# Optimization experiments

Measured on AMD Instinct MI355X. Metric: run time of the kernel, lower is better.

Reference implementation:

```python
import jax, jax.numpy as jnp
import numpy as np

B, N, D, H = 8, 2048, 512, 8  # batch, seq (incl. CLS), emb_dim, heads


def setup_inputs() -> dict:
    key = jax.random.key(0)
    kx, km, k1, k2, k3, k4 = jax.random.split(key, 6)
    x = jax.random.normal(kx, (B, N, D), dtype=jnp.float32)
    # mask covers the N-1 non-CLS tokens; forward pads a leading True for CLS
    mask = jax.random.bernoulli(km, p=0.9, shape=(B, N - 1))
    s = 0.02
    Wqkv = jax.random.normal(k1, (D, 3 * D), dtype=jnp.float32) * s
    bqkv = jax.random.normal(k2, (3 * D,), dtype=jnp.float32) * s
    Wout = jax.random.normal(k3, (D, D), dtype=jnp.float32) * s
    bout = jax.random.normal(k4, (D,), dtype=jnp.float32) * s
    return {"x": x, "mask": mask, "Wqkv": Wqkv, "bqkv": bqkv,
            "Wout": Wout, "bout": bout, "num_heads": H}


def reference(x, mask, Wqkv, bqkv, Wout, bout, num_heads):
    b, n, d = x.shape
    h = num_heads
    dh = d // h
    scale = d ** (-0.5)  # NOTE: module scales by emb_dim^-0.5, not head_dim^-0.5

    qkv = x @ Wqkv + bqkv                      # [b, n, 3d]
    q, k, v = jnp.split(qkv, 3, axis=-1)
    def to_heads(t):
        return t.reshape(b, n, h, dh).transpose(0, 2, 1, 3)  # [b, h, n, dh]
    q, k, v = map(to_heads, (q, k, v))

    scores = jnp.einsum('bhqd,bhkd->bhqk', q, k) * scale     # [b, h, n, n]

    # pad leading True for CLS token, then outer-product pair mask
    m = jnp.pad(mask, ((0, 0), (1, 0)), constant_values=True)  # [b, n]
    pair = m[:, None, :, None] & m[:, None, None, :]           # [b, 1, n, n]
    neg = jnp.asarray(-1e9, dtype=scores.dtype)  # finite stand-in for -inf (avoids NaN rows)
    scores = jnp.where(pair, scores, neg)

    attn = jax.nn.softmax(scores, axis=-1)
    out = jnp.einsum('bhqk,bhkd->bhqd', attn, v)               # [b, h, n, dh]
    out = out.transpose(0, 2, 1, 3).reshape(b, n, d)
    return out @ Wout + bout
```

## Files before the change

### kernel.cpp

```cpp
#include <hip/hip_runtime.h>
#include <math.h>

#define BB  8
#define SEQ 2048
#define EMB 512
#define NH  8
#define DH  64
#define NBH (BB * NH)
#define MROWS (BB * SEQ)
#define QKV_ELEMS ((size_t)NBH * SEQ * DH)
#define MASK_ELEMS (BB * (SEQ - 1))
#define QSCALE 0.06375871307545f

typedef __attribute__((ext_vector_type(8)))  short short8;
typedef __attribute__((ext_vector_type(4)))  float float4e;
typedef __attribute__((ext_vector_type(16))) float float16e;
typedef __attribute__((ext_vector_type(4)))  unsigned int uint4e;
typedef __attribute__((ext_vector_type(2)))  unsigned int uint2e;
typedef unsigned short ushort_t;

static __device__ inline unsigned short f2bf(float f) {
    unsigned int u = __float_as_uint(f);
    unsigned int r = (u + 0x7fffu + ((u >> 16) & 1u)) >> 16;
    return (unsigned short)r;
}

static __device__ inline void gl_lds16(const unsigned short* g, unsigned short* l) {
    __builtin_amdgcn_global_load_lds(
        (const __attribute__((address_space(1))) void*)g,
        (__attribute__((address_space(3))) void*)l, 16, 0, 0);
}

#define PREP_CONV   8192
#define PREP_MASK   (PREP_CONV + 64)
#define PREP_WQ     (PREP_MASK + (1536 / 32) * (EMB / 32))
#define PREP_TOTAL  (PREP_WQ + (EMB / 32) * (EMB / 32))

__global__ __launch_bounds__(256) void prep(const float* __restrict__ x,
                                            const void* __restrict__ mraw,
                                            const float* __restrict__ Wqkv,
                                            const float* __restrict__ Wout,
                                            ushort_t* __restrict__ xb,
                                            float* __restrict__ pmf,
                                            unsigned* __restrict__ pmb,
                                            ushort_t* __restrict__ wqt,
                                            ushort_t* __restrict__ wot) {
    __shared__ float T[32][33];
    __shared__ int flag;
    const int bid = blockIdx.x;
    const int tid = threadIdx.x;

    if (bid < PREP_CONV) {
        const size_t i = ((size_t)bid * 256 + tid) * 4;
        float4 v = *(const float4*)&x[i];
        ushort4 o;
        o.x = f2bf(v.x); o.y = f2bf(v.y); o.z = f2bf(v.z); o.w = f2bf(v.w);
        *(ushort4*)&xb[i] = o;
    } else if (bid < PREP_MASK) {
        if (tid == 0) flag = 0;
        __syncthreads();
        const unsigned int* mi = (const unsigned int*)mraw;
        int local = 0;
        for (int i = tid; i < MASK_ELEMS / 4; i += 256) {
            if (mi[i] > 1u) local = 1;
        }
        if (local) flag = 1;
        __syncthreads();
        const int isbyte = flag;
        const unsigned char* mb = (const unsigned char*)mraw;
        const int* m32 = (const int*)mraw;
        const int i = (bid - PREP_CONV) * 256 + tid;
        const int b = i >> 11, n = i & (SEQ - 1);
        int v;
        if (n == 0) v = 1;
        else {
            const int src = b * (SEQ - 1) + n - 1;
            v = isbyte ? (int)mb[src] : (m32[src] != 0 ? 1 : 0);
        }
        pmf[i] = v ? 1.0f : 0.0f;
        const unsigned long long bl = __ballot(v);
        if ((tid & 31) == 0) pmb[i >> 5] = (unsigned)(bl >> (tid & 32));
    } else {
        const float* src;
        ushort_t* dst;
        int N, idx;
        if (bid < PREP_WQ) {
            src = Wqkv; dst = wqt; N = 1536; idx = bid - PREP_MASK;
        } else {
            src = Wout; dst = wot; N = EMB; idx = bid - PREP_WQ;
        }
        const int nb = N / 32;
        const int n0 = (idx % nb) * 32;
        const int k0 = (idx / nb) * 32;
        {
            const int r = tid >> 3, c4 = (tid & 7) * 4;
            *(float4*)&T[r][c4] = *(const float4*)&src[(size_t)(k0 + r) * N + n0 + c4];
        }
        __syncthreads();
        const int n = tid >> 3, k4 = (tid & 7) * 4;
        ushort4 hv;
        hv.x = f2bf(T[k4 + 0][n]);
        hv.y = f2bf(T[k4 + 1][n]);
        hv.z = f2bf(T[k4 + 2][n]);
        hv.w = f2bf(T[k4 + 3][n]);
        *(ushort4*)&dst[(size_t)(n0 + n) * EMB + k0 + k4] = hv;
    }
}

__global__ __launch_bounds__(256) void qkv_mfma(const ushort_t* __restrict__ xb,
                                                const ushort_t* __restrict__ wt,
                                                const float* __restrict__ bias,
                                                ushort_t* __restrict__ qb,
                                                ushort_t* __restrict__ kb,
                                                ushort_t* __restrict__ vt) {
    __shared__ __align__(16) ushort_t As[128 * 64];
    __shared__ __align__(16) ushort_t Bs[128 * 64];
    const int tid  = threadIdx.x;
    const int w    = tid >> 6;
    const int lane = tid & 63;
    const int l16  = lane & 15;
    const int quad = lane >> 4;
    const int wq   = w >> 1;
    const int wn   = w & 1;
    const int bid  = blockIdx.x;
    const int c    = bid & 7;
    const int r    = bid >> 3;
    const int mloc = r / 12;
    const int nblk = r - mloc * 12;
    const int row0 = (c * 16 + mloc) * 128;
    const int col0 = nblk * 128;

    float4e acc[4][4];
    #pragma unroll
    for (int i = 0; i < 4; ++i)
        #pragma unroll
        for (int j = 0; j < 4; ++j) acc[i][j] = (float4e){0.f, 0.f, 0.f, 0.f};

    const int srow = tid >> 3;
    const int csrc = (tid & 7) ^ (srow & 7);

    for (int k0 = 0; k0 < EMB; k0 += 64) {
        #pragma unroll
        for (int s = 0; s < 4; ++s) {
            const int row = s * 32 + srow;
            gl_lds16(xb + (size_t)(row0 + row) * EMB + k0 + csrc * 8,
                     As + s * 2048 + w * 512);
            gl_lds16(wt + (size_t)(col0 + row) * EMB + k0 + csrc * 8,
                     Bs + s * 2048 + w * 512);
        }
        __syncthreads();
        #pragma unroll
        for (int kk = 0; kk < 2; ++kk) {
            short8 af[4], bf[4];
            #pragma unroll
            for (int mt = 0; mt < 4; ++mt) {
                const int rm = wq * 64 + mt * 16 + l16;
                af[mt] = *(const short8*)(As + rm * 64 + (((kk * 4 + quad) ^ (rm & 7)) * 8));
            }
            #pragma unroll
            for (int nt = 0; nt < 4; ++nt) {
                const int rn = wn * 64 + nt * 16 + l16;
                bf[nt] = *(const short8*)(Bs + rn * 64 + (((kk * 4 + quad) ^ (rn & 7)) * 8));
            }
            #pragma unroll
            for (int mt = 0; mt < 4; ++mt)
                #pragma unroll
                for (int nt = 0; nt < 4; ++nt)
                    acc[mt][nt] = __builtin_amdgcn_mfma_f32_16x16x32_bf16(af[mt], bf[nt], acc[mt][nt], 0, 0, 0);
        }
        __syncthreads();
    }

    #pragma unroll
    for (int nt = 0; nt < 4; ++nt) {
        const int cb    = col0 + wn * 64 + nt * 16;
        const int which = cb >> 9;
        const int h     = (cb >> 6) & 7;
        const int dcol  = (cb & 63) + l16;
        const float bz  = bias[cb + l16];
        if (which == 2) {
            #pragma unroll
            for (int mt = 0; mt < 4; ++mt) {
                const int rg = row0 + wq * 64 + mt * 16 + quad * 4;
                const int b = rg >> 11, n = rg & (SEQ - 1);
                ushort4 ov;
                ov.x = f2bf(acc[mt][nt][0] + bz);
                ov.y = f2bf(acc[mt][nt][1] + bz);
                ov.z = f2bf(acc[mt][nt][2] + bz);
                ov.w = f2bf(acc[mt][nt][3] + bz);
                *(ushort4*)&vt[((size_t)(b * NH + h) * DH + dcol) * SEQ + n] = ov;
            }
        } else {
            ushort_t* base = (which == 0) ? qb : kb;
            const float sc = (which == 0) ? QSCALE : 1.0f;
            #pragma unroll
            for (int mt = 0; mt < 4; ++mt) {
                #pragma unroll
                for (int i = 0; i < 4; ++i) {
                    const int rg = row0 + wq * 64 + mt * 16 + quad * 4 + i;
                    const int b = rg >> 11;
                    const int n = rg & (SEQ - 1);
                    base[((size_t)(b * NH + h) * SEQ + n) * DH + dcol] =
                        f2bf((acc[mt][nt][i] + bz) * sc);
                }
            }
        }
    }
}

__global__ __launch_bounds__(64, 2) void attn_mfma(const ushort_t* __restrict__ qb,
                                                   const ushort_t* __restrict__ kb,
                                                   const ushort_t* __restrict__ vt,
                                                   const float* __restrict__ pmf,
                                                   const unsigned* __restrict__ pmb,
                                                   ushort_t* __restrict__ ab) {
    __shared__ __align__(16) ushort_t Ks0[32 * 64];
    __shared__ __align__(16) ushort_t Vs0[64 * 32];
    __shared__ __align__(16) ushort_t Ks1[32 * 64];
    __shared__ __align__(16) ushort_t Vs1[64 * 32];
    __shared__ float lw[64];

    const int lane = threadIdx.x;
    const int l5   = lane & 31;
    const int h    = lane >> 5;
    const int bid = blockIdx.x;
    const int ord = bid >> 3;
    const int bh  = (bid & 7) * 8 + (ord >> 5);
    const int qt  = ord & 31;
    const int b   = bh >> 3;
    const int hh  = bh & 7;
    const int q0  = qt * 64;

    const ushort_t* qbh = qb + (size_t)bh * SEQ * DH;
    short8 qf[2][4];
    #pragma unroll
    for (int t = 0; t < 2; ++t)
        #pragma unroll
        for (int kc = 0; kc < 4; ++kc)
            qf[t][kc] = *(const short8*)(qbh + (size_t)(q0 + t * 32 + l5) * DH + kc * 16 + h * 8);

    bool qv[2];
    #pragma unroll
    for (int t = 0; t < 2; ++t) {
        const float mq = pmf[b * SEQ + q0 + t * 32 + l5];
        qv[t] = (mq != 0.0f);
        if (!qv[t]) {
            const short8 z8 = {0, 0, 0, 0, 0, 0, 0, 0};
            #pragma unroll
            for (int kc = 0; kc < 4; ++kc) qf[t][kc] = z8;
        }
    }

    const unsigned wm = pmb[b * 64 + lane];

    const ushort_t* kbh = kb + (size_t)bh * SEQ * DH;
    const ushort_t* vbh = vt + (size_t)bh * DH * SEQ;

    const int l3  = lane >> 3;
    const int c8  = (lane & 7) ^ (l3 & 7);
    const int l2  = lane >> 2;
    const int c4v = (lane & 3) ^ (l2 & 3);

    float16e o[2][2];
    #pragma unroll
    for (int t = 0; t < 2; ++t)
        #pragma unroll
        for (int d = 0; d < 2; ++d) o[t][d] = (float16e)0.0f;
    float l_i[2] = {0.f, 0.f};

    auto stage = [&](int kt, ushort_t* Kd, ushort_t* Vd) {
        #pragma unroll
        for (int j = 0; j < 4; ++j) {
            gl_lds16(kbh + (size_t)(kt * 32 + j * 8 + l3) * DH + c8 * 8, Kd + j * 512);
            gl_lds16(vbh + (size_t)(j * 16 + l2) * SEQ + kt * 32 + c4v * 8, Vd + j * 512);
        }
    };

    auto body = [&](int kt, const ushort_t* Kr, const ushort_t* Vr,
                    ushort_t* Kw, ushort_t* Vw) {
        stage(kt + 1, Kw, Vw);
        asm volatile("s_waitcnt vmcnt(8)" ::: "memory");
        __builtin_amdgcn_sched_barrier(0);

        const unsigned mwf = (unsigned)__builtin_amdgcn_readlane((int)wm, kt);
        const unsigned mh  = h ? (mwf >> 4) : mwf;
        float16e st0, st1;
        #pragma unroll
        for (int j = 0; j < 16; ++j) {
            const float bv = (mh & (1u << ((j & 3) + 8 * (j >> 2)))) ? 0.0f : -1e9f;
            st0[j] = qv[0] ? bv : 0.0f;
            st1[j] = qv[1] ? bv : 0.0f;
        }

        short8 kf[4];
        #pragma unroll
        for (int kc = 0; kc < 4; ++kc)
            kf[kc] = *(const short8*)(Kr + l5 * 64 + (((kc * 2 + h) ^ (l5 & 7)) * 8));
        __builtin_amdgcn_s_setprio(1);
        #pragma unroll
        for (int kc = 0; kc < 4; ++kc) {
            st0 = __builtin_amdgcn_mfma_f32_32x32x16_bf16(kf[kc], qf[0][kc], st0, 0, 0, 0);
            st1 = __builtin_amdgcn_mfma_f32_32x32x16_bf16(kf[kc], qf[1][kc], st1, 0, 0, 0);
        }
        __builtin_amdgcn_s_setprio(0);

        short8 af[2][2];
        #pragma unroll
        for (int t = 0; t < 2; ++t) {
            const float16e& st = t ? st1 : st0;
            unsigned int a[8];
            float lacc = 0.f;
            #pragma unroll
            for (int j = 0; j < 8; ++j) {
                const float p0 = __builtin_amdgcn_exp2f(st[2 * j]);
                const float p1 = __builtin_amdgcn_exp2f(st[2 * j + 1]);
                lacc += p0 + p1;
                a[j] = (__float_as_uint(p0) >> 16) | (__float_as_uint(p1) & 0xffff0000u);
            }
            l_i[t] += lacc;
            #pragma unroll
            for (int c = 0; c < 2; ++c) {
                const uint2e r02 = __builtin_amdgcn_permlane32_swap(a[4 * c],     a[4 * c + 2], false, false);
                const uint2e r13 = __builtin_amdgcn_permlane32_swap(a[4 * c + 1], a[4 * c + 3], false, false);
                uint4e fv;
                fv.x = r02[0];
                fv.y = r13[0];
                fv.z = r02[1];
                fv.w = r13[1];
                af[t][c] = __builtin_bit_cast(short8, fv);
            }
        }

        __builtin_amdgcn_s_setprio(1);
        #pragma unroll
        for (int c = 0; c < 2; ++c) {
            #pragma unroll
            for (int d = 0; d < 2; ++d) {
                const int vr = d * 32 + l5;
                const short8 vf = *(const short8*)(Vr + vr * 32 +
                                   (((c * 2 + h) ^ (vr & 3)) * 8));
                o[0][d] = __builtin_amdgcn_mfma_f32_32x32x16_bf16(af[0][c], vf, o[0][d], 0, 0, 0);
                o[1][d] = __builtin_amdgcn_mfma_f32_32x32x16_bf16(af[1][c], vf, o[1][d], 0, 0, 0);
            }
        }
        __builtin_amdgcn_s_setprio(0);
    };

    stage(0, Ks0, Vs0);
    for (int kt2 = 0; kt2 < 64; kt2 += 2) {
        body(kt2,     Ks0, Vs0, Ks1, Vs1);
        body(kt2 + 1, Ks1, Vs1, Ks0, Vs0);
    }

    #pragma unroll
    for (int t = 0; t < 2; ++t) {
        const float l = l_i[t] + __shfl_xor(l_i[t], 32);
        lw[t * 32 + l5] = l;
    }

    ushort_t* ob = ab + ((size_t)b * SEQ + q0) * EMB + hh * DH;
    #pragma unroll
    for (int t = 0; t < 2; ++t) {
        #pragma unroll
        for (int r = 0; r < 16; ++r) {
            const int ql = (r & 3) + 8 * (r >> 2) + 4 * h;
            const float inv = 1.0f / lw[t * 32 + ql];
            #pragma unroll
            for (int d = 0; d < 2; ++d)
                ob[(size_t)(t * 32 + ql) * EMB + d * 32 + l5] = f2bf(o[t][d][r] * inv);
        }
    }
}

__global__ __launch_bounds__(256) void out_mfma(const ushort_t* __restrict__ ab,
                                                const ushort_t* __restrict__ wot,
                                                const float* __restrict__ bias,
                                                float* __restrict__ out) {
    __shared__ __align__(16) ushort_t As[128 * 64];
    __shared__ __align__(16) ushort_t Bs[128 * 64];
    const int tid  = threadIdx.x;
    const int w    = tid >> 6;
    const int lane = tid & 63;
    const int l16  = lane & 15;
    const int quad = lane >> 4;
    const int wq   = w >> 1;
    const int wn   = w & 1;
    const int bid  = blockIdx.x;
    const int c    = bid & 7;
    const int r    = bid >> 3;
    const int mloc = r >> 2;
    const int nblk = r & 3;
    const int row0 = (c * 16 + mloc) * 128;
    const int col0 = nblk * 128;

    float4e acc[4][4];
    #pragma unroll
    for (int i = 0; i < 4; ++i)
        #pragma unroll
        for (int j = 0; j < 4; ++j) acc[i][j] = (float4e){0.f, 0.f, 0.f, 0.f};

    const int srow = tid >> 3;
    const int csrc = (tid & 7) ^ (srow & 7);

    for (int k0 = 0; k0 < EMB; k0 += 64) {
        #pragma unroll
        for (int s = 0; s < 4; ++s) {
            const int row = s * 32 + srow;
            gl_lds16(ab + (size_t)(row0 + row) * EMB + k0 + csrc * 8,
                     As + s * 2048 + w * 512);
            gl_lds16(wot + (size_t)(col0 + row) * EMB + k0 + csrc * 8,
                     Bs + s * 2048 + w * 512);
        }
        __syncthreads();
        #pragma unroll
        for (int kk = 0; kk < 2; ++kk) {
            short8 af[4], bf[4];
            #pragma unroll
            for (int mt = 0; mt < 4; ++mt) {
                const int rm = wq * 64 + mt * 16 + l16;
                af[mt] = *(const short8*)(As + rm * 64 + (((kk * 4 + quad) ^ (rm & 7)) * 8));
            }
            #pragma unroll
            for (int nt = 0; nt < 4; ++nt) {
                const int rn = wn * 64 + nt * 16 + l16;
                bf[nt] = *(const short8*)(Bs + rn * 64 + (((kk * 4 + quad) ^ (rn & 7)) * 8));
            }
            #pragma unroll
            for (int mt = 0; mt < 4; ++mt)
                #pragma unroll
                for (int nt = 0; nt < 4; ++nt)
                    acc[mt][nt] = __builtin_amdgcn_mfma_f32_16x16x32_bf16(af[mt], bf[nt], acc[mt][nt], 0, 0, 0);
        }
        __syncthreads();
    }

    #pragma unroll
    for (int nt = 0; nt < 4; ++nt) {
        const int col_g = col0 + wn * 64 + nt * 16 + l16;
        const float bz = bias[col_g];
        #pragma unroll
        for (int mt = 0; mt < 4; ++mt) {
            #pragma unroll
            for (int i = 0; i < 4; ++i) {
                const int row_g = row0 + wq * 64 + mt * 16 + quad * 4 + i;
                out[(size_t)row_g * EMB + col_g] = acc[mt][nt][i] + bz;
            }
        }
    }
}

extern "C" void kernel_launch(void* const* d_in, const int* in_sizes, int n_in,
                              void* d_out, int out_size, void* d_ws, size_t ws_size,
                              hipStream_t stream) {
    const float* x    = (const float*)d_in[0];
    const void*  mask = d_in[1];
    const float* Wqkv = (const float*)d_in[2];
    const float* bqkv = (const float*)d_in[3];
    const float* Wout = (const float*)d_in[4];
    const float* bout = (const float*)d_in[5];
    float* out = (float*)d_out;

    ushort_t* xb  = (ushort_t*)d_ws;
    ushort_t* wqt = xb + (size_t)MROWS * EMB;
    ushort_t* wot = wqt + (size_t)1536 * EMB;
    ushort_t* qb  = wot + (size_t)EMB * EMB;
    ushort_t* kb  = qb + QKV_ELEMS;
    ushort_t* vt  = kb + QKV_ELEMS;
    ushort_t* ab  = vt + QKV_ELEMS;
    float*    pmf = (float*)(ab + (size_t)MROWS * EMB);
    unsigned* pmb = (unsigned*)(pmf + (size_t)BB * SEQ);

    prep<<<dim3(PREP_TOTAL), 256, 0, stream>>>(x, mask, Wqkv, Wout, xb, pmf, pmb, wqt, wot);
    qkv_mfma<<<dim3(1536), 256, 0, stream>>>(xb, wqt, bqkv, qb, kb, vt);
    attn_mfma<<<dim3(NBH * (SEQ / 64)), 64, 0, stream>>>(qb, kb, vt, pmf, pmb, ab);
    out_mfma<<<dim3(512), 256, 0, stream>>>(ab, wot, bout, out);
}
```

Baseline: 247.1 us.

## Halve attention query tile and software-pipeline QK^T with softmax·V across iterations

```diff
diff --git a/kernel.cpp b/kernel.cpp
--- a/kernel.cpp
+++ b/kernel.cpp
@@ -215,40 +215,34 @@
                                                    const unsigned* __restrict__ pmb,
                                                    ushort_t* __restrict__ ab) {
     __shared__ __align__(16) ushort_t Ks0[32 * 64];
+    __shared__ __align__(16) ushort_t Ks1[32 * 64];
     __shared__ __align__(16) ushort_t Vs0[64 * 32];
-    __shared__ __align__(16) ushort_t Ks1[32 * 64];
     __shared__ __align__(16) ushort_t Vs1[64 * 32];
-    __shared__ float lw[64];
+    __shared__ float lw[32];
 
     const int lane = threadIdx.x;
     const int l5   = lane & 31;
     const int h    = lane >> 5;
     const int bid = blockIdx.x;
     const int ord = bid >> 3;
-    const int bh  = (bid & 7) * 8 + (ord >> 5);
-    const int qt  = ord & 31;
+    const int bh  = (bid & 7) * 8 + (ord >> 6);
+    const int qt  = ord & 63;
     const int b   = bh >> 3;
     const int hh  = bh & 7;
-    const int q0  = qt * 64;
+    const int q0  = qt * 32;
 
     const ushort_t* qbh = qb + (size_t)bh * SEQ * DH;
-    short8 qf[2][4];
+    short8 qf[4];
     #pragma unroll
-    for (int t = 0; t < 2; ++t)
-        #pragma unroll
-        for (int kc = 0; kc < 4; ++kc)
-            qf[t][kc] = *(const short8*)(qbh + (size_t)(q0 + t * 32 + l5) * DH + kc * 16 + h * 8);
-
-    bool qv[2];
-    #pragma unroll
-    for (int t = 0; t < 2; ++t) {
-        const float mq = pmf[b * SEQ + q0 + t * 32 + l5];
-        qv[t] = (mq != 0.0f);
-        if (!qv[t]) {
-            const short8 z8 = {0, 0, 0, 0, 0, 0, 0, 0};
-            #pragma unroll
-            for (int kc = 0; kc < 4; ++kc) qf[t][kc] = z8;
-        }
+    for (int kc = 0; kc < 4; ++kc)
+        qf[kc] = *(const short8*)(qbh + (size_t)(q0 + l5) * DH + kc * 16 + h * 8);
+
+    const float mq = pmf[b * SEQ + q0 + l5];
+    const bool qv = (mq != 0.0f);
+    if (!qv) {
+        const short8 z8 = {0, 0, 0, 0, 0, 0, 0, 0};
+        #pragma unroll
+        for (int kc = 0; kc < 4; ++kc) qf[kc] = z8;
     }
 
     const unsigned wm = pmb[b * 64 + lane];
@@ -259,14 +253,12 @@
     const int l3  = lane >> 3;
     const int c8  = (lane & 7) ^ (l3 & 7);
     const int l2  = lane >> 2;
-    const int c4v = (lane & 3) ^ (l2 & 3);
-
-    float16e o[2][2];
-    #pragma unroll
-    for (int t = 0; t < 2; ++t)
-        #pragma unroll
-        for (int d = 0; d < 2; ++d) o[t][d] = (float16e)0.0f;
-    float l_i[2] = {0.f, 0.f};
+    const int c4v = (lane & 3) ^ ((lane >> 2) & 3) ^ ((lane >> 4) & 3);
+
+    float16e o[2];
+    o[0] = (float16e)0.0f;
+    o[1] = (float16e)0.0f;
+    float l_i = 0.f;
 
     auto stage = [&](int kt, ushort_t* Kd, ushort_t* Vd) {
         #pragma unroll
@@ -276,100 +268,160 @@
         }
     };
 
-    auto body = [&](int kt, const ushort_t* Kr, const ushort_t* Vr,
-                    ushort_t* Kw, ushort_t* Vw) {
-        stage(kt + 1, Kw, Vw);
-        asm volatile("s_waitcnt vmcnt(8)" ::: "memory");
+    float16e stE, stO;
+
+#define ABODY(KT, KC, KO, VO, STP, STC)                                        \
+    {                                                                          \
+        asm volatile("s_waitcnt vmcnt(0)" ::: "memory");        \
+        short8 vf[2][2];                                                       \
+        _Pragma("unroll")                                                      \
+        for (int c = 0; c < 2; ++c)                                            \
+            _Pragma("unroll")                                                  \
+            for (int d = 0; d < 2; ++d) {                                      \
+                const int vr = d * 32 + l5;                                    \
+                vf[c][d] = *(const short8*)((VO) + vr * 32 +                   \
+                    (((c * 2 + h) ^ (vr & 3) ^ ((vr >> 2) & 3)) * 8));         \
+            }                                                                  \
+        short8 kf[4];                                                          \
+        _Pragma("unroll")                                                      \
+        for (int kc = 0; kc < 4; ++kc)                                         \
+            kf[kc] = *(const short8*)((KC) + l5 * 64 +                         \
+                       (((kc * 2 + h) ^ (l5 & 7)) * 8));                       \
+        asm volatile("s_waitcnt lgkmcnt(0)" ::: "memory");                     \
+        __builtin_amdgcn_sched_barrier(0);                                     \
+        stage((KT) + 1, (KO), (VO));               \
+                  \
+        {                                                                      \
+            const unsigned mwf = (unsigned)__builtin_amdgcn_readlane((int)wm, (KT)); \
+            const unsigned mh = h ? (mwf >> 4) : mwf;                          \
+            _Pragma("unroll")                                                  \
+            for (int j = 0; j < 16; ++j) {                                     \
+                const float bv = (mh & (1u << ((j & 3) + 8 * (j >> 2)))) ? 0.0f : -1e9f; \
+                (STC)[j] = qv ? bv : 0.0f;                                     \
+            }                                                                  \
+            __builtin_amdgcn_s_setprio(1);                                     \
+            _Pragma("unroll")                                                  \
+            for (int kc = 0; kc < 4; ++kc)                                     \
+                (STC) = __builtin_amdgcn_mfma_f32_32x32x16_bf16(kf[kc], qf[kc], (STC), 0, 0, 0); \
+            __builtin_amdgcn_s_setprio(0);                                     \
+        }                                                                      \
+                           \
+        short8 af[2];                                                          \
+        {                                                                      \
+            unsigned int a[8];                                                 \
+            float lacc = 0.f;                                                  \
+            _Pragma("unroll")                                                  \
+            for (int j = 0; j < 8; ++j) {                                      \
+                const float p0 = __builtin_amdgcn_exp2f((STP)[2 * j]);         \
+                const float p1 = __builtin_amdgcn_exp2f((STP)[2 * j + 1]);     \
+                lacc += p0 + p1;                                               \
+                a[j] = (__float_as_uint(p0) >> 16) | (__float_as_uint(p1) & 0xffff0000u); \
+            }                                                                  \
+            l_i += lacc;                                                       \
+            _Pragma("unroll")                                                  \
+            for (int c = 0; c < 2; ++c) {                                      \
+                const uint2e r02 = __builtin_amdgcn_permlane32_swap(a[4 * c],     a[4 * c + 2], false, false); \
+                const uint2e r13 = __builtin_amdgcn_permlane32_swap(a[4 * c + 1], a[4 * c + 3], false, false); \
+                uint4e fv;                                                     \
+                fv.x = r02[0];                                                 \
+                fv.y = r13[0];                                                 \
+                fv.z = r02[1];                                                 \
+                fv.w = r13[1];                                                 \
+                af[c] = __builtin_bit_cast(short8, fv);                        \
+            }                                                                  \
+        }                                                                      \
+                                                                 \
+        __builtin_amdgcn_s_setprio(1);                                         \
+        _Pragma("unroll")                                                      \
+        for (int c = 0; c < 2; ++c)                                            \
+            _Pragma("unroll")                                                  \
+            for (int d = 0; d < 2; ++d)                                        \
+                o[d] = __builtin_amdgcn_mfma_f32_32x32x16_bf16(af[c], vf[c][d], o[d], 0, 0, 0); \
+        __builtin_amdgcn_s_setprio(0);                                         \
+    }
+
+    stage(0, Ks0, Vs0);
+    asm volatile("s_waitcnt vmcnt(0)" ::: "memory");
+    stage(1, Ks1, Vs1);
+    {
+        short8 kf[4];
+        #pragma unroll
+        for (int kc = 0; kc < 4; ++kc)
+            kf[kc] = *(const short8*)(Ks0 + l5 * 64 + (((kc * 2 + h) ^ (l5 & 7)) * 8));
+        asm volatile("s_waitcnt lgkmcnt(0)" ::: "memory");
         __builtin_amdgcn_sched_barrier(0);
-
-        const unsigned mwf = (unsigned)__builtin_amdgcn_readlane((int)wm, kt);
-        const unsigned mh  = h ? (mwf >> 4) : mwf;
-        float16e st0, st1;
+        const unsigned mwf = (unsigned)__builtin_amdgcn_readlane((int)wm, 0);
+        const unsigned mh = h ? (mwf >> 4) : mwf;
         #pragma unroll
         for (int j = 0; j < 16; ++j) {
             const float bv = (mh & (1u << ((j & 3) + 8 * (j >> 2)))) ? 0.0f : -1e9f;
-            st0[j] = qv[0] ? bv : 0.0f;
-            st1[j] = qv[1] ? bv : 0.0f;
-        }
-
-        short8 kf[4];
+            stE[j] = qv ? bv : 0.0f;
+        }
         #pragma unroll
         for (int kc = 0; kc < 4; ++kc)
-            kf[kc] = *(const short8*)(Kr + l5 * 64 + (((kc * 2 + h) ^ (l5 & 7)) * 8));
-        __builtin_amdgcn_s_setprio(1);
-        #pragma unroll
-        for (int kc = 0; kc < 4; ++kc) {
-            st0 = __builtin_amdgcn_mfma_f32_32x32x16_bf16(kf[kc], qf[0][kc], st0, 0, 0, 0);
-            st1 = __builtin_amdgcn_mfma_f32_32x32x16_bf16(kf[kc], qf[1][kc], st1, 0, 0, 0);
-        }
-        __builtin_amdgcn_s_setprio(0);
-
-        short8 af[2][2];
-        #pragma unroll
-        for (int t = 0; t < 2; ++t) {
-            const float16e& st = t ? st1 : st0;
-            unsigned int a[8];
-            float lacc = 0.f;
-            #pragma unroll
-            for (int j = 0; j < 8; ++j) {
-                const float p0 = __builtin_amdgcn_exp2f(st[2 * j]);
-                const float p1 = __builtin_amdgcn_exp2f(st[2 * j + 1]);
-                lacc += p0 + p1;
-                a[j] = (__float_as_uint(p0) >> 16) | (__float_as_uint(p1) & 0xffff0000u);
-            }
-            l_i[t] += lacc;
-            #pragma unroll
-            for (int c = 0; c < 2; ++c) {
-                const uint2e r02 = __builtin_amdgcn_permlane32_swap(a[4 * c],     a[4 * c + 2], false, false);
-                const uint2e r13 = __builtin_amdgcn_permlane32_swap(a[4 * c + 1], a[4 * c + 3], false, false);
-                uint4e fv;
-                fv.x = r02[0];
-                fv.y = r13[0];
-                fv.z = r02[1];
-                fv.w = r13[1];
-                af[t][c] = __builtin_bit_cast(short8, fv);
-            }
-        }
-
-        __builtin_amdgcn_s_setprio(1);
-        #pragma unroll
-        for (int c = 0; c < 2; ++c) {
+            stE = __builtin_amdgcn_mfma_f32_32x32x16_bf16(kf[kc], qf[kc], stE, 0, 0, 0);
+    }
+
+    for (int kt2 = 1; kt2 < 63; kt2 += 2) {
+        ABODY(kt2,     Ks1, Ks0, Vs0, stE, stO)
+        ABODY(kt2 + 1, Ks0, Ks1, Vs1, stO, stE)
+    }
+    ABODY(63, Ks1, Ks0, Vs0, stE, stO)
+
+    {
+        short8 vf[2][2];
+        #pragma unroll
+        for (int c = 0; c < 2; ++c)
             #pragma unroll
             for (int d = 0; d < 2; ++d) {
                 const int vr = d * 32 + l5;
-                const short8 vf = *(const short8*)(Vr + vr * 32 +
-                                   (((c * 2 + h) ^ (vr & 3)) * 8));
-                o[0][d] = __builtin_amdgcn_mfma_f32_32x32x16_bf16(af[0][c], vf, o[0][d], 0, 0, 0);
-                o[1][d] = __builtin_amdgcn_mfma_f32_32x32x16_bf16(af[1][c], vf, o[1][d], 0, 0, 0);
-            }
-        }
-        __builtin_amdgcn_s_setprio(0);
-    };
-
-    stage(0, Ks0, Vs0);
-    for (int kt2 = 0; kt2 < 64; kt2 += 2) {
-        body(kt2,     Ks0, Vs0, Ks1, Vs1);
-        body(kt2 + 1, Ks1, Vs1, Ks0, Vs0);
-    }
-
-    #pragma unroll
-    for (int t = 0; t < 2; ++t) {
-        const float l = l_i[t] + __shfl_xor(l_i[t], 32);
-        lw[t * 32 + l5] = l;
+                vf[c][d] = *(const short8*)(Vs1 + vr * 32 +
+                    (((c * 2 + h) ^ (vr & 3) ^ ((vr >> 2) & 3)) * 8));
+            }
+        unsigned int a[8];
+        float lacc = 0.f;
+        #pragma unroll
+        for (int j = 0; j < 8; ++j) {
+            const float p0 = __builtin_amdgcn_exp2f(stO[2 * j]);
+            const float p1 = __builtin_amdgcn_exp2f(stO[2 * j + 1]);
+            lacc += p0 + p1;
+            a[j] = (__float_as_uint(p0) >> 16) | (__float_as_uint(p1) & 0xffff0000u);
+        }
+        l_i += lacc;
+        short8 af[2];
+        #pragma unroll
+        for (int c = 0; c < 2; ++c) {
+            const uint2e r02 = __builtin_amdgcn_permlane32_swap(a[4 * c],     a[4 * c + 2], false, false);
+            const uint2e r13 = __builtin_amdgcn_permlane32_swap(a[4 * c + 1], a[4 * c + 3], false, false);
+            uint4e fv;
+            fv.x = r02[0];
+            fv.y = r13[0];
+            fv.z = r02[1];
+            fv.w = r13[1];
+            af[c] = __builtin_bit_cast(short8, fv);
+        }
+        #pragma unroll
+        for (int c = 0; c < 2; ++c)
+            #pragma unroll
+            for (int d = 0; d < 2; ++d)
+                o[d] = __builtin_amdgcn_mfma_f32_32x32x16_bf16(af[c], vf[c][d], o[d], 0, 0, 0);
+    }
+
+    {
+        const float l = l_i + __shfl_xor(l_i, 32);
+        lw[l5] = l;
     }
 
     ushort_t* ob = ab + ((size_t)b * SEQ + q0) * EMB + hh * DH;
     #pragma unroll
-    for (int t = 0; t < 2; ++t) {
-        #pragma unroll
-        for (int r = 0; r < 16; ++r) {
-            const int ql = (r & 3) + 8 * (r >> 2) + 4 * h;
-            const float inv = 1.0f / lw[t * 32 + ql];
-            #pragma unroll
-            for (int d = 0; d < 2; ++d)
-                ob[(size_t)(t * 32 + ql) * EMB + d * 32 + l5] = f2bf(o[t][d][r] * inv);
-        }
-    }
+    for (int r = 0; r < 16; ++r) {
+        const int ql = (r & 3) + 8 * (r >> 2) + 4 * h;
+        const float inv = 1.0f / lw[ql];
+        #pragma unroll
+        for (int d = 0; d < 2; ++d)
+            ob[(size_t)ql * EMB + d * 32 + l5] = f2bf(o[d][r] * inv);
+    }
+#undef ABODY
 }
 
 __global__ __launch_bounds__(256) void out_mfma(const ushort_t* __restrict__ ab,
@@ -472,6 +524,6 @@
 
     prep<<<dim3(PREP_TOTAL), 256, 0, stream>>>(x, mask, Wqkv, Wout, xb, pmf, pmb, wqt, wot);
     qkv_mfma<<<dim3(1536), 256, 0, stream>>>(xb, wqt, bqkv, qb, kb, vt);
-    attn_mfma<<<dim3(NBH * (SEQ / 64)), 64, 0, stream>>>(qb, kb, vt, pmf, pmb, ab);
+    attn_mfma<<<dim3(NBH * (SEQ / 32)), 64, 0, stream>>>(qb, kb, vt, pmf, pmb, ab);
     out_mfma<<<dim3(512), 256, 0, stream>>>(ab, wot, bout, out);
 }
```

Measured after the change: 282.0 us. 1.14x slower.
